# Optimization experiments

Measured on AMD Instinct MI355X. Metric: run time of the kernel, lower is better.

Reference implementation:

```python
import jax, jax.numpy as jnp
import numpy as np

B, S, D, H = 8, 2048, 1024, 8
CHUNK = D // H
SCALE = float(D) ** (-0.5)  # key_dim ** -0.5, key_dim == num_units here
LN_EPS = 1e-5


def setup_inputs() -> dict:
    key = jax.random.key(0)
    ks = jax.random.split(key, 9)
    s = 0.02
    return {
        "query": jax.random.normal(ks[0], (B, S, D), jnp.float32),
        "keys": jax.random.normal(ks[1], (B, S, D), jnp.float32),
        "Wq": jax.random.normal(ks[2], (D, D), jnp.float32) * s,  # torch Linear weight [out,in]
        "Wk": jax.random.normal(ks[3], (D, D), jnp.float32) * s,
        "Wv": jax.random.normal(ks[4], (D, D), jnp.float32) * s,
        "Wp": jax.random.normal(ks[5], (D, D), jnp.float32) * s,
        "bp": jnp.zeros((D,), jnp.float32),
        "ln_gamma": jnp.ones((D,), jnp.float32),
        "ln_beta": jnp.zeros((D,), jnp.float32),
    }


def reference(query, keys, Wq, Wk, Wv, Wp, bp, ln_gamma, ln_beta):
    # Linear layers (no bias on q/k/v): y = x @ W.T
    Q = jnp.einsum("bsd,ed->bse", query, Wq)
    K = jnp.einsum("bsd,ed->bse", keys, Wk)
    V = jnp.einsum("bsd,ed->bse", keys, Wv)
    # Faithful to original: raw view to [B*h, S, chunk] (no transpose head split)
    Qh = Q.reshape(B * H, S, CHUNK)
    Kh = K.reshape(B * H, S, CHUNK)
    Vh = V.reshape(B * H, S, CHUNK)
    # scores [B*h, S, S], scale, softmax (is_masked=False, dropout_p=0)
    att = jnp.einsum("gqc,gkc->gqk", Qh, Kh) * SCALE
    att = jax.nn.softmax(att, axis=-1)
    ctx = jnp.einsum("gqk,gkc->gqc", att, Vh).reshape(B, S, D)
    # output projection + residual + LayerNorm
    out = jnp.einsum("bsd,ed->bse", ctx, Wp) + bp
    out = out + query
    mu = jnp.mean(out, axis=-1, keepdims=True)
    var = jnp.mean(jnp.square(out - mu), axis=-1, keepdims=True)
    out = (out - mu) * jax.lax.rsqrt(var + LN_EPS) * ln_gamma + ln_beta
    return out
```

## Files before the change

kernel.cpp:

```cpp
#include <hip/hip_runtime.h>

typedef __bf16 bf16x8 __attribute__((ext_vector_type(8)));
typedef float f32x4 __attribute__((ext_vector_type(4)));
typedef float f32x16 __attribute__((ext_vector_type(16)));
typedef unsigned uint2e __attribute__((ext_vector_type(2)));

#define SCLOG 0.04508422f

__device__ __forceinline__ unsigned short f2bf(float f) {
  union { float f; unsigned int u; } v;
  v.f = f;
  unsigned int u = v.u;
  u += 0x7fffu + ((u >> 16) & 1u);
  return (unsigned short)(u >> 16);
}

__device__ __forceinline__ void gld_lds16(const void* g, void* l) {
  __builtin_amdgcn_global_load_lds(
      (const __attribute__((address_space(1))) void*)g,
      (__attribute__((address_space(3))) void*)l, 16, 0, 0);
}

__global__ __launch_bounds__(256) void convert_kernel(
    const float* __restrict__ q, const float* __restrict__ k,
    const float* __restrict__ wq, const float* __restrict__ wk,
    const float* __restrict__ wv, const float* __restrict__ wp,
    unsigned short* __restrict__ qb, unsigned short* __restrict__ kb,
    unsigned short* __restrict__ Wqkv, unsigned short* __restrict__ Wpb) {
  size_t i = (size_t)blockIdx.x * 256 + threadIdx.x;
  const float* src; unsigned short* dst; size_t off;
  if (i < 4194304)      { src = q;  dst = qb;             off = i; }
  else if (i < 8388608) { src = k;  dst = kb;             off = i - 4194304; }
  else if (i < 8650752) { src = wq; dst = Wqkv;           off = i - 8388608; }
  else if (i < 8912896) { src = wk; dst = Wqkv + 1048576; off = i - 8650752; }
  else if (i < 9175040) { src = wv; dst = Wqkv + 2097152; off = i - 8912896; }
  else                  { src = wp; dst = Wpb;            off = i - 9175040; }
  float4 v = ((const float4*)src)[off];
  ushort4 o;
  o.x = f2bf(v.x); o.y = f2bf(v.y); o.z = f2bf(v.z); o.w = f2bf(v.w);
  ((ushort4*)dst)[off] = o;
}

#define QKV_BAR __builtin_amdgcn_s_barrier()
#define QKV_LGKM asm volatile("s_waitcnt lgkmcnt(0)" ::: "memory")

#define QKV_STG(lc, h, srcb, s)                                               \
  gld_lds16((srcb) + (size_t)(s) * 128 + gro0, (lc) + (h) * 16384 + d0);      \
  gld_lds16((srcb) + (size_t)(s) * 128 + gro1, (lc) + (h) * 16384 + d0 + 1024);

#define QKV_RDA(I0)                                                           \
  _Pragma("unroll") for (int i4 = 0; i4 < 4; ++i4) {                          \
    af[i4][0] = *(const bf16x8*)(tb + rbA + ((I0) + i4) * 2048 + cx0);        \
    af[i4][1] = *(const bf16x8*)(tb + rbA + ((I0) + i4) * 2048 + cx1);        \
  }

#define QKV_RDB(JP)                                                           \
  _Pragma("unroll") for (int j2 = 0; j2 < 2; ++j2) {                          \
    bfr[JP][j2][0] = *(const bf16x8*)(tb + rbB + ((JP) * 2 + j2) * 2048 + cx0); \
    bfr[JP][j2][1] = *(const bf16x8*)(tb + rbB + ((JP) * 2 + j2) * 2048 + cx1); \
  }

#define QKV_MM(I0, JP)                                                        \
  _Pragma("unroll") for (int i4 = 0; i4 < 4; ++i4)                            \
  _Pragma("unroll") for (int j2 = 0; j2 < 2; ++j2)                            \
  _Pragma("unroll") for (int kk = 0; kk < 2; ++kk)                            \
    acc[(I0) + i4][(JP) * 2 + j2] = __builtin_amdgcn_mfma_f32_16x16x32_bf16(  \
        af[i4][kk], bfr[JP][j2][kk], acc[(I0) + i4][(JP) * 2 + j2], 0, 0, 0);

__global__ __launch_bounds__(512, 2) void gemm_qkv8_kernel(
    const unsigned short* __restrict__ qb,
    const unsigned short* __restrict__ kb,
    const unsigned short* __restrict__ W,
    unsigned short* __restrict__ Qo,
    unsigned short* __restrict__ Ko,
    unsigned short* __restrict__ Vo) {
  __shared__ char lds[131072];

  const int t = threadIdx.x;
  const int lane = t & 63;
  const int w = t >> 6;
  const int fr = lane & 15;
  const int quad = lane >> 4;

  const int orig = blockIdx.x;
  const int sseq = orig >> 3;
  const int tn = sseq >> 3;
  const int tm = (orig & 7) * 8 + (sseq & 7);

  const unsigned short* Ap = (tn < 4) ? qb : kb;
  const char* aBase = (const char*)Ap + (size_t)(tm * 256) * 2048;
  const char* bBase = (const char*)W + (size_t)(tn * 256) * 2048;

  const int wm2 = w >> 2, wn4 = w & 3;

  const size_t gro0 = (size_t)(w * 16 + (lane >> 3)) * 2048 + (size_t)(((lane & 7) ^ (lane >> 3)) << 4);
  const size_t gro1 = gro0 + 8 * 2048;
  const int d0 = w * 2048 + lane * 16;

  const int rbA = (wm2 * 128 + fr) * 128;
  const int rbB = 32768 + (wn4 * 64 + fr) * 128;
  const int cx0 = (quad * 16) ^ ((fr & 7) << 4);
  const int cx1 = cx0 ^ 64;

  f32x4 acc[8][4];
#pragma unroll
  for (int i = 0; i < 8; ++i)
#pragma unroll
    for (int j = 0; j < 4; ++j) acc[i][j] = (f32x4){0.f, 0.f, 0.f, 0.f};

#pragma unroll
  for (int s = 0; s < 2; ++s) {
    char* lc = lds + s * 65536;
    QKV_STG(lc, 0, aBase, s);
    QKV_STG(lc, 1, aBase + 262144, s);
    QKV_STG(lc + 32768, 0, bBase, s);
    QKV_STG(lc + 32768, 1, bBase + 262144, s);
  }
  asm volatile("s_waitcnt vmcnt(8)" ::: "memory");
  QKV_BAR;

#pragma unroll 1
  for (int kt = 0; kt < 16; ++kt) {
    const char* tb = lds + (kt & 1) * 65536;
    char* lc = lds + (kt & 1) * 65536;
    const int s = kt + 2;
    bf16x8 af[4][2], bfr[2][2][2];

    QKV_RDA(0);
    QKV_RDB(0);
    QKV_BAR; QKV_LGKM;
    __builtin_amdgcn_s_setprio(1);
    QKV_MM(0, 0);
    __builtin_amdgcn_s_setprio(0);
    QKV_BAR;

    QKV_RDB(1);
    QKV_BAR; QKV_LGKM;
    __builtin_amdgcn_s_setprio(1);
    QKV_MM(0, 1);
    __builtin_amdgcn_s_setprio(0);
    QKV_BAR;

    QKV_RDA(4);
    if (s < 16) {
      QKV_STG(lc + 32768, 0, bBase, s);
      QKV_STG(lc + 32768, 1, bBase + 262144, s);
    }
    QKV_BAR; QKV_LGKM;
    __builtin_amdgcn_s_setprio(1);
    QKV_MM(4, 1);
    __builtin_amdgcn_s_setprio(0);
    QKV_BAR;

    if (s < 16) {
      QKV_STG(lc, 0, aBase, s);
      QKV_STG(lc, 1, aBase + 262144, s);
    }
    QKV_BAR;
    __builtin_amdgcn_s_setprio(1);
    QKV_MM(4, 0);
    __builtin_amdgcn_s_setprio(0);
    if (kt <= 13)      { asm volatile("s_waitcnt vmcnt(8)" ::: "memory"); }
    else if (kt == 14) { asm volatile("s_waitcnt vmcnt(0)" ::: "memory"); }
    if (kt < 15) QKV_BAR;
  }

  const int sel = tn >> 2;
  unsigned short* Out = sel == 0 ? Qo : (sel == 1 ? Ko : Vo);
  const float osc = (sel == 0) ? SCLOG : 1.f;
  const int row0 = tm * 256 + wm2 * 128 + quad * 4;
  const int col0 = (tn & 3) * 256 + wn4 * 64 + fr;
#pragma unroll
  for (int i = 0; i < 8; ++i)
#pragma unroll
    for (int j = 0; j < 4; ++j)
#pragma unroll
      for (int r = 0; r < 4; ++r)
        Out[(size_t)(row0 + i * 16 + r) * 1024 + col0 + j * 16] = f2bf(acc[i][j][r] * osc);
}

__global__ __launch_bounds__(256) void vtrans_kernel(
    const unsigned short* __restrict__ V, unsigned short* __restrict__ Vt) {
  __shared__ unsigned short T[128 * 136];
  const int g  = blockIdx.x >> 4;
  const int kt = blockIdx.x & 15;
  const unsigned short* Vg = V + (size_t)g * 262144 + (size_t)kt * 128 * 128;
  unsigned short* Vtg = Vt + (size_t)g * 262144 + kt * 128;
  const int t = threadIdx.x;
#pragma unroll
  for (int it = 0; it < 8; it++) {
    int seg = t + it * 256;
    int k  = seg >> 4;
    int c8 = (seg & 15) << 3;
    uint4 a = *(const uint4*)(Vg + k * 128 + c8);
    unsigned short* Tp = &T[c8 * 136 + k];
    Tp[0 * 136] = (unsigned short)(a.x & 0xffff);
    Tp[1 * 136] = (unsigned short)(a.x >> 16);
    Tp[2 * 136] = (unsigned short)(a.y & 0xffff);
    Tp[3 * 136] = (unsigned short)(a.y >> 16);
    Tp[4 * 136] = (unsigned short)(a.z & 0xffff);
    Tp[5 * 136] = (unsigned short)(a.z >> 16);
    Tp[6 * 136] = (unsigned short)(a.w & 0xffff);
    Tp[7 * 136] = (unsigned short)(a.w >> 16);
  }
  __syncthreads();
#pragma unroll
  for (int it = 0; it < 8; it++) {
    int seg = t + it * 256;
    int c  = seg >> 4;
    int k8 = (seg & 15) << 3;
    uint4 o = *(const uint4*)&T[c * 136 + k8];
    *(uint4*)(Vtg + (size_t)c * 2048 + k8) = o;
  }
}

#define PACK_HALF(EX, KSBASE)                                                  \
    _Pragma("unroll")                                                          \
    for (int c2 = 0; c2 < 2; c2++)                                             \
      _Pragma("unroll")                                                        \
      for (int e = 0; e < 2; e++) {                                            \
        unsigned ua, ub;                                                       \
        asm("v_cvt_pk_bf16_f32 %0, %1, %2" : "=v"(ua)                          \
            : "v"(EX[8 * c2 + 2 * e]), "v"(EX[8 * c2 + 2 * e + 1]));           \
        asm("v_cvt_pk_bf16_f32 %0, %1, %2" : "=v"(ub)                          \
            : "v"(EX[8 * c2 + 4 + 2 * e]), "v"(EX[8 * c2 + 4 + 2 * e + 1]));   \
        uint2e rr = __builtin_amdgcn_permlane32_swap(ua, ub, false, false);    \
        if (e == 0) { paw[(KSBASE) + c2].x = rr[0]; paw[(KSBASE) + c2].z = rr[1]; } \
        else        { paw[(KSBASE) + c2].y = rr[0]; paw[(KSBASE) + c2].w = rr[1]; } \
      }

#define ATTN_TILE(KSH, VSH, KST, VST, PREF)                                    \
  {                                                                            \
    if (PREF) {                                                                \
      gld_lds16(kp + kS0, (KST) + kD0);                                        \
      gld_lds16(kp + kS1, (KST) + kD1);                                        \
      gld_lds16(vp + vS0, (VST) + vD0);                                        \
      gld_lds16(vp + vS1, (VST) + vD1);                                        \
      kp += 8192; vp += 64;                                                    \
    }                                                                          \
    f32x16 s0, s1;                                                             \
    _Pragma("unroll")                                                          \
    for (int r = 0; r < 16; r++) { s0[r] = 0.f; s1[r] = 0.f; }                 \
    {                                                                          \
      bf16x8 kf[8];                                                            \
      _Pragma("unroll")                                                        \
      for (int ks = 0; ks < 8; ks++)                                           \
        kf[ks] = *(const bf16x8*)((KSH) + kb0 + kOf[ks]);                      \
      _Pragma("unroll")                                                        \
      for (int ks = 0; ks < 8; ks++)                                           \
        s0 = __builtin_amdgcn_mfma_f32_32x32x16_bf16(kf[ks], qf[ks], s0, 0, 0, 0); \
    }                                                                          \
    {                                                                          \
      bf16x8 kf[8];                                                            \
      _Pragma("unroll")                                                        \
      for (int ks = 0; ks < 8; ks++)                                           \
        kf[ks] = *(const bf16x8*)((KSH) + kb0 + 8192 + kOf[ks]);               \
      _Pragma("unroll")                                                        \
      for (int ks = 0; ks < 8; ks++)                                           \
        s1 = __builtin_amdgcn_mfma_f32_32x32x16_bf16(kf[ks], qf[ks], s1, 0, 0, 0); \
    }                                                                          \
    float ex0[16], ex1[16];                                                    \
    _Pragma("unroll")                                                          \
    for (int r = 0; r < 16; r++) {                                             \
      ex0[r] = __builtin_amdgcn_exp2f(fminf(s0[r], 30.f));                     \
      ex1[r] = __builtin_amdgcn_exp2f(fminf(s1[r], 30.f));                     \
      lp += ex0[r] + ex1[r];                                                   \
    }                                                                          \
    uint4 paw[4];                                                              \
    PACK_HALF(ex0, 0)                                                          \
    PACK_HALF(ex1, 2)                                                          \
    _Pragma("unroll")                                                          \
    for (int cb = 0; cb < 4; cb++) {                                           \
      _Pragma("unroll")                                                        \
      for (int ks = 0; ks < 4; ks++) {                                         \
        bf16x8 vf = *(const bf16x8*)((VSH) + cb * 4096 + vOf[ks]);             \
        bf16x8 pa8 = __builtin_bit_cast(bf16x8, paw[ks]);                      \
        O[cb] = __builtin_amdgcn_mfma_f32_32x32x16_bf16(pa8, vf, O[cb], 0, 0, 0); \
      }                                                                        \
    }                                                                          \
    __syncthreads();                                                           \
  }

__global__ __launch_bounds__(512, 1) void attn_kernel(
    const unsigned short* __restrict__ Q,
    const unsigned short* __restrict__ K,
    const unsigned short* __restrict__ Vt,
    unsigned short* __restrict__ ctx) {
  __shared__ unsigned char smem[65536];

  const int bid = blockIdx.x;
  const int g  = (bid & 7) * 8 + (bid >> 6);
  const int qt = (bid >> 3) & 7;
  const unsigned short* Qg = Q + (size_t)g * 262144 + (size_t)qt * 32768;
  const unsigned short* Kg = K + (size_t)g * 262144;
  const unsigned short* Vg = Vt + (size_t)g * 262144;

  const int t    = threadIdx.x;
  const int lane = t & 63;
  const int wv   = t >> 6;
  const int col  = lane & 31;
  const int hi   = lane >> 5;
  const int qrow = wv * 32 + col;

  int kOf[8];
#pragma unroll
  for (int ks = 0; ks < 8; ks++) {
    int c = ks * 2 + hi;
    kOf[ks] = ((c & 8) | ((c ^ (col & 7)) & 7)) << 4;
  }
  const int kb0 = col * 256;
  int vOf[4];
#pragma unroll
  for (int ks = 0; ks < 4; ks++) {
    int c = ks * 2 + hi;
    vOf[ks] = col * 128 + (((c ^ (col & 7)) & 7) << 4);
  }
  int kS0, kS1, kD0, kD1, vS0, vS1, vD0, vD1;
  {
    int seg0 = t, seg1 = t + 512;
    int r0 = seg0 >> 4, p0 = seg0 & 15, c0 = (p0 & 8) | ((p0 ^ r0) & 7);
    int r1 = seg1 >> 4, p1 = seg1 & 15, c1 = (p1 & 8) | ((p1 ^ r1) & 7);
    kS0 = r0 * 128 + c0 * 8;  kD0 = seg0 * 16;
    kS1 = r1 * 128 + c1 * 8;  kD1 = seg1 * 16;
    int vr0 = seg0 >> 3, vp0 = seg0 & 7, vc0 = vp0 ^ (vr0 & 7);
    int vr1 = seg1 >> 3, vp1 = seg1 & 7, vc1 = vp1 ^ (vr1 & 7);
    vS0 = vr0 * 2048 + vc0 * 8;  vD0 = seg0 * 16;
    vS1 = vr1 * 2048 + vc1 * 8;  vD1 = seg1 * 16;
  }

#pragma unroll
  for (int it = 0; it < 8; it++) {
    int seg = t + it * 512;
    int r = seg >> 4, p = seg & 15;
    int c = (p & 8) | ((p ^ r) & 7);
    gld_lds16(Qg + r * 128 + c * 8, smem + seg * 16);
  }
  __syncthreads();
  bf16x8 qf[8];
#pragma unroll
  for (int ks = 0; ks < 8; ks++) {
    int c = ks * 2 + hi;
    int p = (c & 8) | ((c ^ (qrow & 7)) & 7);
    qf[ks] = *(const bf16x8*)(smem + qrow * 256 + p * 16);
  }
  __syncthreads();

  gld_lds16(Kg + kS0, smem + kD0);
  gld_lds16(Kg + kS1, smem + kD1);
  gld_lds16(Vg + vS0, smem + 32768 + vD0);
  gld_lds16(Vg + vS1, smem + 32768 + vD1);
  __syncthreads();

  const unsigned short* kp = Kg + 8192;
  const unsigned short* vp = Vg + 64;

  f32x16 O[4];
#pragma unroll
  for (int cb = 0; cb < 4; cb++)
#pragma unroll
    for (int r = 0; r < 16; r++) O[cb][r] = 0.f;
  float lp = 0.f;

  unsigned char* B0K = smem;
  unsigned char* B1K = smem + 16384;
  unsigned char* B0V = smem + 32768;
  unsigned char* B1V = smem + 49152;

#pragma unroll 1
  for (int kt2 = 0; kt2 < 16; kt2++) {
    ATTN_TILE(B0K, B0V, B1K, B1V, 1);
    ATTN_TILE(B1K, B1V, B0K, B0V, (kt2 < 15));
  }

  lp += __shfl_xor(lp, 32);
  float* linv_arr = (float*)smem;
  linv_arr[wv * 32 + col] = 1.f / lp;
  float4 li[4];
#pragma unroll
  for (int rq = 0; rq < 4; rq++)
    li[rq] = *(const float4*)&linv_arr[wv * 32 + rq * 8 + hi * 4];

  unsigned short* Cg = ctx + (size_t)g * 262144 + (size_t)qt * 32768;
#pragma unroll
  for (int cb = 0; cb < 4; cb++)
#pragma unroll
    for (int rq = 0; rq < 4; rq++)
#pragma unroll
      for (int j = 0; j < 4; j++) {
        int row = wv * 32 + rq * 8 + hi * 4 + j;
        Cg[(size_t)row * 128 + cb * 32 + col] = f2bf(O[cb][rq * 4 + j] * li[rq][j]);
      }
}

__global__ __launch_bounds__(256) void gemm_proj_kernel(
    const unsigned short* __restrict__ A,
    const unsigned short* __restrict__ W,
    const float* __restrict__ bp,
    const float* __restrict__ qres,
    float* __restrict__ out) {
  __shared__ unsigned short Alds[128 * 32];
  __shared__ unsigned short Blds[128 * 32];
  const int t   = threadIdx.x;
  const int bid = blockIdx.x;
  const int tn  = bid % 8;
  const int tm  = bid / 8;
  const unsigned short* Bptr = W + (size_t)tn * 128 * 1024;

  const int lane = t & 63;
  const int wv   = t >> 6;
  const int wm   = (wv >> 1) * 64;
  const int wn   = (wv & 1) * 64;
  const int fr   = lane & 15;
  const int kq   = (lane >> 4) * 8;

  f32x4 acc[4][4];
#pragma unroll
  for (int i = 0; i < 4; i++)
#pragma unroll
    for (int j = 0; j < 4; j++) acc[i][j] = (f32x4){0.f, 0.f, 0.f, 0.f};

  const int sr = t >> 2;
  const int sc = (t & 3) << 3;
  const unsigned short* gA = A + (size_t)(tm * 128 + sr) * 1024 + sc;
  const unsigned short* gB = Bptr + (size_t)sr * 1024 + sc;
  unsigned short* lA = Alds + t * 8;
  unsigned short* lB = Blds + t * 8;

  for (int k0 = 0; k0 < 1024; k0 += 32) {
    gld_lds16(gA, lA);
    gld_lds16(gA + 64 * 1024, lA + 64 * 32);
    gld_lds16(gB, lB);
    gld_lds16(gB + 64 * 1024, lB + 64 * 32);
    gA += 32; gB += 32;
    __syncthreads();
    bf16x8 af[4], bfr[4];
#pragma unroll
    for (int i = 0; i < 4; i++) {
      af[i]  = *(const bf16x8*)&Alds[(wm + i * 16 + fr) * 32 + kq];
      bfr[i] = *(const bf16x8*)&Blds[(wn + i * 16 + fr) * 32 + kq];
    }
#pragma unroll
    for (int i = 0; i < 4; i++)
#pragma unroll
      for (int j = 0; j < 4; j++)
        acc[i][j] = __builtin_amdgcn_mfma_f32_16x16x32_bf16(af[i], bfr[j], acc[i][j], 0, 0, 0);
    __syncthreads();
  }

  const int quad = lane >> 4;
  const int cc   = lane & 15;
#pragma unroll
  for (int i = 0; i < 4; i++)
#pragma unroll
    for (int j = 0; j < 4; j++)
#pragma unroll
      for (int r = 0; r < 4; r++) {
        int row = tm * 128 + wm + i * 16 + quad * 4 + r;
        int col = tn * 128 + wn + j * 16 + cc;
        out[(size_t)row * 1024 + col] =
            acc[i][j][r] + bp[col] + qres[(size_t)row * 1024 + col];
      }
}

__global__ __launch_bounds__(256) void ln_kernel(float* __restrict__ out,
                                                 const float* __restrict__ gamma,
                                                 const float* __restrict__ beta) {
  __shared__ float red[8];
  const int row = blockIdx.x;
  float* p = out + (size_t)row * 1024;
  const int t = threadIdx.x;
  float4 v = ((const float4*)p)[t];
  float s  = v.x + v.y + v.z + v.w;
  float s2 = v.x * v.x + v.y * v.y + v.z * v.z + v.w * v.w;
#pragma unroll
  for (int off = 1; off < 64; off <<= 1) {
    s  += __shfl_xor(s, off);
    s2 += __shfl_xor(s2, off);
  }
  const int wv = t >> 6;
  if ((t & 63) == 0) { red[wv] = s; red[4 + wv] = s2; }
  __syncthreads();
  float S  = red[0] + red[1] + red[2] + red[3];
  float S2 = red[4] + red[5] + red[6] + red[7];
  float mu  = S * (1.f / 1024.f);
  float var = S2 * (1.f / 1024.f) - mu * mu;
  float rstd = rsqrtf(var + 1e-5f);
  float4 gm = ((const float4*)gamma)[t];
  float4 bt = ((const float4*)beta)[t];
  v.x = (v.x - mu) * rstd * gm.x + bt.x;
  v.y = (v.y - mu) * rstd * gm.y + bt.y;
  v.z = (v.z - mu) * rstd * gm.z + bt.z;
  v.w = (v.w - mu) * rstd * gm.w + bt.w;
  ((float4*)p)[t] = v;
}

extern "C" void kernel_launch(void* const* d_in, const int* in_sizes, int n_in,
                              void* d_out, int out_size, void* d_ws, size_t ws_size,
                              hipStream_t stream) {
  const float* query = (const float*)d_in[0];
  const float* keys  = (const float*)d_in[1];
  const float* Wq    = (const float*)d_in[2];
  const float* Wk    = (const float*)d_in[3];
  const float* Wv    = (const float*)d_in[4];
  const float* Wp    = (const float*)d_in[5];
  const float* bp    = (const float*)d_in[6];
  const float* gamma = (const float*)d_in[7];
  const float* beta  = (const float*)d_in[8];
  float* out = (float*)d_out;

  unsigned short* ws   = (unsigned short*)d_ws;
  unsigned short* qb   = ws;
  unsigned short* kb   = ws + 16777216;
  unsigned short* Wqkv = ws + 33554432;
  unsigned short* Wpb  = ws + 36700160;
  unsigned short* Qb   = ws + 37748736;
  unsigned short* Kb   = ws + 54525952;
  unsigned short* Vb   = ws + 71303168;
  unsigned short* Vtb  = kb;
  unsigned short* ctx  = qb;

  convert_kernel<<<36864, 256, 0, stream>>>(query, keys, Wq, Wk, Wv, Wp, qb, kb, Wqkv, Wpb);
  gemm_qkv8_kernel<<<768, 512, 0, stream>>>(qb, kb, Wqkv, Qb, Kb, Vb);
  vtrans_kernel<<<1024, 256, 0, stream>>>(Vb, Vtb);
  attn_kernel<<<512, 512, 0, stream>>>(Qb, Kb, Vtb, ctx);
  gemm_proj_kernel<<<1024, 256, 0, stream>>>(ctx, Wpb, bp, query, out);
  ln_kernel<<<16384, 256, 0, stream>>>(out, gamma, beta);
}
```

Before: 523.7 us.

## Reuse pipelined 256x256 QKV GEMM for output projection; widen attention LDS swizzle

Result: faster. 507.1 us (-3.2%).

```diff
diff --git a/kernel.cpp b/kernel.cpp
--- a/kernel.cpp
+++ b/kernel.cpp
@@ -67,6 +67,75 @@
     acc[(I0) + i4][(JP) * 2 + j2] = __builtin_amdgcn_mfma_f32_16x16x32_bf16(  \
         af[i4][kk], bfr[JP][j2][kk], acc[(I0) + i4][(JP) * 2 + j2], 0, 0, 0);
 
+#define QKV_KLOOP                                                             \
+  _Pragma("unroll")                                                           \
+  for (int s = 0; s < 2; ++s) {                                               \
+    char* lc = lds + s * 65536;                                               \
+    QKV_STG(lc, 0, aBase, s);                                                 \
+    QKV_STG(lc, 1, aBase + 262144, s);                                        \
+    QKV_STG(lc + 32768, 0, bBase, s);                                         \
+    QKV_STG(lc + 32768, 1, bBase + 262144, s);                                \
+  }                                                                           \
+  asm volatile("s_waitcnt vmcnt(8)" ::: "memory");                            \
+  QKV_BAR;                                                                    \
+  _Pragma("unroll 1")                                                         \
+  for (int kt = 0; kt < 16; ++kt) {                                           \
+    const char* tb = lds + (kt & 1) * 65536;                                  \
+    char* lc = lds + (kt & 1) * 65536;                                        \
+    const int s = kt + 2;                                                     \
+    bf16x8 af[4][2], bfr[2][2][2];                                            \
+    QKV_RDA(0);                                                               \
+    QKV_RDB(0);                                                               \
+    QKV_BAR; QKV_LGKM;                                                        \
+    __builtin_amdgcn_s_setprio(1);                                            \
+    QKV_MM(0, 0);                                                             \
+    __builtin_amdgcn_s_setprio(0);                                            \
+    QKV_BAR;                                                                  \
+    QKV_RDB(1);                                                               \
+    QKV_BAR; QKV_LGKM;                                                        \
+    __builtin_amdgcn_s_setprio(1);                                            \
+    QKV_MM(0, 1);                                                             \
+    __builtin_amdgcn_s_setprio(0);                                            \
+    QKV_BAR;                                                                  \
+    QKV_RDA(4);                                                               \
+    if (s < 16) {                                                             \
+      QKV_STG(lc + 32768, 0, bBase, s);                                       \
+      QKV_STG(lc + 32768, 1, bBase + 262144, s);                              \
+    }                                                                         \
+    QKV_BAR; QKV_LGKM;                                                        \
+    __builtin_amdgcn_s_setprio(1);                                            \
+    QKV_MM(4, 1);                                                             \
+    __builtin_amdgcn_s_setprio(0);                                            \
+    QKV_BAR;                                                                  \
+    if (s < 16) {                                                             \
+      QKV_STG(lc, 0, aBase, s);                                               \
+      QKV_STG(lc, 1, aBase + 262144, s);                                      \
+    }                                                                         \
+    QKV_BAR;                                                                  \
+    __builtin_amdgcn_s_setprio(1);                                            \
+    QKV_MM(4, 0);                                                             \
+    __builtin_amdgcn_s_setprio(0);                                            \
+    if (kt <= 13)      { asm volatile("s_waitcnt vmcnt(8)" ::: "memory"); }   \
+    else if (kt == 14) { asm volatile("s_waitcnt vmcnt(0)" ::: "memory"); }   \
+    if (kt < 15) QKV_BAR;                                                     \
+  }
+
+#define QKV_COMMON_DECLS                                                      \
+  const int t = threadIdx.x;                                                  \
+  const int lane = t & 63;                                                    \
+  const int w = t >> 6;                                                       \
+  const int fr = lane & 15;                                                   \
+  const int quad = lane >> 4;                                                 \
+  const int wm2 = w >> 2, wn4 = w & 3;                                        \
+  const size_t gro0 = (size_t)(w * 16 + (lane >> 3)) * 2048 +                 \
+                      (size_t)(((lane & 7) ^ (lane >> 3)) << 4);              \
+  const size_t gro1 = gro0 + 8 * 2048;                                        \
+  const int d0 = w * 2048 + lane * 16;                                        \
+  const int rbA = (wm2 * 128 + fr) * 128;                                     \
+  const int rbB = 32768 + (wn4 * 64 + fr) * 128;                              \
+  const int cx0 = (quad * 16) ^ ((fr & 7) << 4);                              \
+  const int cx1 = cx0 ^ 64;
+
 __global__ __launch_bounds__(512, 2) void gemm_qkv8_kernel(
     const unsigned short* __restrict__ qb,
     const unsigned short* __restrict__ kb,
@@ -75,12 +144,7 @@
     unsigned short* __restrict__ Ko,
     unsigned short* __restrict__ Vo) {
   __shared__ char lds[131072];
-
-  const int t = threadIdx.x;
-  const int lane = t & 63;
-  const int w = t >> 6;
-  const int fr = lane & 15;
-  const int quad = lane >> 4;
+  QKV_COMMON_DECLS
 
   const int orig = blockIdx.x;
   const int sseq = orig >> 3;
@@ -91,79 +155,13 @@
   const char* aBase = (const char*)Ap + (size_t)(tm * 256) * 2048;
   const char* bBase = (const char*)W + (size_t)(tn * 256) * 2048;
 
-  const int wm2 = w >> 2, wn4 = w & 3;
-
-  const size_t gro0 = (size_t)(w * 16 + (lane >> 3)) * 2048 + (size_t)(((lane & 7) ^ (lane >> 3)) << 4);
-  const size_t gro1 = gro0 + 8 * 2048;
-  const int d0 = w * 2048 + lane * 16;
-
-  const int rbA = (wm2 * 128 + fr) * 128;
-  const int rbB = 32768 + (wn4 * 64 + fr) * 128;
-  const int cx0 = (quad * 16) ^ ((fr & 7) << 4);
-  const int cx1 = cx0 ^ 64;
-
   f32x4 acc[8][4];
 #pragma unroll
   for (int i = 0; i < 8; ++i)
 #pragma unroll
     for (int j = 0; j < 4; ++j) acc[i][j] = (f32x4){0.f, 0.f, 0.f, 0.f};
 
-#pragma unroll
-  for (int s = 0; s < 2; ++s) {
-    char* lc = lds + s * 65536;
-    QKV_STG(lc, 0, aBase, s);
-    QKV_STG(lc, 1, aBase + 262144, s);
-    QKV_STG(lc + 32768, 0, bBase, s);
-    QKV_STG(lc + 32768, 1, bBase + 262144, s);
-  }
-  asm volatile("s_waitcnt vmcnt(8)" ::: "memory");
-  QKV_BAR;
-
-#pragma unroll 1
-  for (int kt = 0; kt < 16; ++kt) {
-    const char* tb = lds + (kt & 1) * 65536;
-    char* lc = lds + (kt & 1) * 65536;
-    const int s = kt + 2;
-    bf16x8 af[4][2], bfr[2][2][2];
-
-    QKV_RDA(0);
-    QKV_RDB(0);
-    QKV_BAR; QKV_LGKM;
-    __builtin_amdgcn_s_setprio(1);
-    QKV_MM(0, 0);
-    __builtin_amdgcn_s_setprio(0);
-    QKV_BAR;
-
-    QKV_RDB(1);
-    QKV_BAR; QKV_LGKM;
-    __builtin_amdgcn_s_setprio(1);
-    QKV_MM(0, 1);
-    __builtin_amdgcn_s_setprio(0);
-    QKV_BAR;
-
-    QKV_RDA(4);
-    if (s < 16) {
-      QKV_STG(lc + 32768, 0, bBase, s);
-      QKV_STG(lc + 32768, 1, bBase + 262144, s);
-    }
-    QKV_BAR; QKV_LGKM;
-    __builtin_amdgcn_s_setprio(1);
-    QKV_MM(4, 1);
-    __builtin_amdgcn_s_setprio(0);
-    QKV_BAR;
-
-    if (s < 16) {
-      QKV_STG(lc, 0, aBase, s);
-      QKV_STG(lc, 1, aBase + 262144, s);
-    }
-    QKV_BAR;
-    __builtin_amdgcn_s_setprio(1);
-    QKV_MM(4, 0);
-    __builtin_amdgcn_s_setprio(0);
-    if (kt <= 13)      { asm volatile("s_waitcnt vmcnt(8)" ::: "memory"); }
-    else if (kt == 14) { asm volatile("s_waitcnt vmcnt(0)" ::: "memory"); }
-    if (kt < 15) QKV_BAR;
-  }
+  QKV_KLOOP
 
   const int sel = tn >> 2;
   unsigned short* Out = sel == 0 ? Qo : (sel == 1 ? Ko : Vo);
@@ -177,6 +175,47 @@
 #pragma unroll
       for (int r = 0; r < 4; ++r)
         Out[(size_t)(row0 + i * 16 + r) * 1024 + col0 + j * 16] = f2bf(acc[i][j][r] * osc);
+}
+
+__global__ __launch_bounds__(512, 2) void gemm_proj8_kernel(
+    const unsigned short* __restrict__ A,
+    const unsigned short* __restrict__ W,
+    const float* __restrict__ bp,
+    const float* __restrict__ qres,
+    float* __restrict__ out) {
+  __shared__ char lds[131072];
+  QKV_COMMON_DECLS
+
+  const int orig = blockIdx.x;
+  const int sseq = orig >> 3;
+  const int tn = sseq >> 3;
+  const int tm = (orig & 7) * 8 + (sseq & 7);
+
+  const char* aBase = (const char*)A + (size_t)(tm * 256) * 2048;
+  const char* bBase = (const char*)W + (size_t)(tn * 256) * 2048;
+
+  f32x4 acc[8][4];
+#pragma unroll
+  for (int i = 0; i < 8; ++i)
+#pragma unroll
+    for (int j = 0; j < 4; ++j) acc[i][j] = (f32x4){0.f, 0.f, 0.f, 0.f};
+
+  QKV_KLOOP
+
+  const int row0 = tm * 256 + wm2 * 128 + quad * 4;
+  const int col0 = tn * 256 + wn4 * 64 + fr;
+#pragma unroll
+  for (int i = 0; i < 8; ++i)
+#pragma unroll
+    for (int j = 0; j < 4; ++j) {
+      const int col = col0 + j * 16;
+      const float bpc = bp[col];
+#pragma unroll
+      for (int r = 0; r < 4; ++r) {
+        const size_t idx = (size_t)(row0 + i * 16 + r) * 1024 + col;
+        out[idx] = acc[i][j][r] + bpc + qres[idx];
+      }
+    }
 }
 
 __global__ __launch_bounds__(256) void vtrans_kernel(
@@ -306,33 +345,33 @@
 #pragma unroll
   for (int ks = 0; ks < 8; ks++) {
     int c = ks * 2 + hi;
-    kOf[ks] = ((c & 8) | ((c ^ (col & 7)) & 7)) << 4;
+    kOf[ks] = (c ^ (col & 15)) << 4;
   }
   const int kb0 = col * 256;
   int vOf[4];
 #pragma unroll
   for (int ks = 0; ks < 4; ks++) {
     int c = ks * 2 + hi;
-    vOf[ks] = col * 128 + (((c ^ (col & 7)) & 7) << 4);
+    vOf[ks] = col * 128 + (((c ^ (col & 7) ^ ((col >> 3) & 1)) & 7) << 4);
   }
   int kS0, kS1, kD0, kD1, vS0, vS1, vD0, vD1;
   {
     int seg0 = t, seg1 = t + 512;
-    int r0 = seg0 >> 4, p0 = seg0 & 15, c0 = (p0 & 8) | ((p0 ^ r0) & 7);
-    int r1 = seg1 >> 4, p1 = seg1 & 15, c1 = (p1 & 8) | ((p1 ^ r1) & 7);
-    kS0 = r0 * 128 + c0 * 8;  kD0 = seg0 * 16;
-    kS1 = r1 * 128 + c1 * 8;  kD1 = seg1 * 16;
-    int vr0 = seg0 >> 3, vp0 = seg0 & 7, vc0 = vp0 ^ (vr0 & 7);
-    int vr1 = seg1 >> 3, vp1 = seg1 & 7, vc1 = vp1 ^ (vr1 & 7);
-    vS0 = vr0 * 2048 + vc0 * 8;  vD0 = seg0 * 16;
-    vS1 = vr1 * 2048 + vc1 * 8;  vD1 = seg1 * 16;
+    int r0 = seg0 >> 4, p0 = seg0 & 15;
+    int r1 = seg1 >> 4, p1 = seg1 & 15;
+    kS0 = r0 * 128 + (p0 ^ (r0 & 15)) * 8;  kD0 = seg0 * 16;
+    kS1 = r1 * 128 + (p1 ^ (r1 & 15)) * 8;  kD1 = seg1 * 16;
+    int vr0 = seg0 >> 3, vp0 = seg0 & 7;
+    int vr1 = seg1 >> 3, vp1 = seg1 & 7;
+    vS0 = vr0 * 2048 + ((vp0 ^ (vr0 & 7) ^ ((vr0 >> 3) & 1)) & 7) * 8;  vD0 = seg0 * 16;
+    vS1 = vr1 * 2048 + ((vp1 ^ (vr1 & 7) ^ ((vr1 >> 3) & 1)) & 7) * 8;  vD1 = seg1 * 16;
   }
 
 #pragma unroll
   for (int it = 0; it < 8; it++) {
     int seg = t + it * 512;
     int r = seg >> 4, p = seg & 15;
-    int c = (p & 8) | ((p ^ r) & 7);
+    int c = p ^ (r & 15);
     gld_lds16(Qg + r * 128 + c * 8, smem + seg * 16);
   }
   __syncthreads();
@@ -340,7 +379,7 @@
 #pragma unroll
   for (int ks = 0; ks < 8; ks++) {
     int c = ks * 2 + hi;
-    int p = (c & 8) | ((c ^ (qrow & 7)) & 7);
+    int p = c ^ (qrow & 15);
     qf[ks] = *(const bf16x8*)(smem + qrow * 256 + p * 16);
   }
   __syncthreads();
@@ -389,76 +428,6 @@
       for (int j = 0; j < 4; j++) {
         int row = wv * 32 + rq * 8 + hi * 4 + j;
         Cg[(size_t)row * 128 + cb * 32 + col] = f2bf(O[cb][rq * 4 + j] * li[rq][j]);
-      }
-}
-
-__global__ __launch_bounds__(256) void gemm_proj_kernel(
-    const unsigned short* __restrict__ A,
-    const unsigned short* __restrict__ W,
-    const float* __restrict__ bp,
-    const float* __restrict__ qres,
-    float* __restrict__ out) {
-  __shared__ unsigned short Alds[128 * 32];
-  __shared__ unsigned short Blds[128 * 32];
-  const int t   = threadIdx.x;
-  const int bid = blockIdx.x;
-  const int tn  = bid % 8;
-  const int tm  = bid / 8;
-  const unsigned short* Bptr = W + (size_t)tn * 128 * 1024;
-
-  const int lane = t & 63;
-  const int wv   = t >> 6;
-  const int wm   = (wv >> 1) * 64;
-  const int wn   = (wv & 1) * 64;
-  const int fr   = lane & 15;
-  const int kq   = (lane >> 4) * 8;
-
-  f32x4 acc[4][4];
-#pragma unroll
-  for (int i = 0; i < 4; i++)
-#pragma unroll
-    for (int j = 0; j < 4; j++) acc[i][j] = (f32x4){0.f, 0.f, 0.f, 0.f};
-
-  const int sr = t >> 2;
-  const int sc = (t & 3) << 3;
-  const unsigned short* gA = A + (size_t)(tm * 128 + sr) * 1024 + sc;
-  const unsigned short* gB = Bptr + (size_t)sr * 1024 + sc;
-  unsigned short* lA = Alds + t * 8;
-  unsigned short* lB = Blds + t * 8;
-
-  for (int k0 = 0; k0 < 1024; k0 += 32) {
-    gld_lds16(gA, lA);
-    gld_lds16(gA + 64 * 1024, lA + 64 * 32);
-    gld_lds16(gB, lB);
-    gld_lds16(gB + 64 * 1024, lB + 64 * 32);
-    gA += 32; gB += 32;
-    __syncthreads();
-    bf16x8 af[4], bfr[4];
-#pragma unroll
-    for (int i = 0; i < 4; i++) {
-      af[i]  = *(const bf16x8*)&Alds[(wm + i * 16 + fr) * 32 + kq];
-      bfr[i] = *(const bf16x8*)&Blds[(wn + i * 16 + fr) * 32 + kq];
-    }
-#pragma unroll
-    for (int i = 0; i < 4; i++)
-#pragma unroll
-      for (int j = 0; j < 4; j++)
-        acc[i][j] = __builtin_amdgcn_mfma_f32_16x16x32_bf16(af[i], bfr[j], acc[i][j], 0, 0, 0);
-    __syncthreads();
-  }
-
-  const int quad = lane >> 4;
-  const int cc   = lane & 15;
-#pragma unroll
-  for (int i = 0; i < 4; i++)
-#pragma unroll
-    for (int j = 0; j < 4; j++)
-#pragma unroll
-      for (int r = 0; r < 4; r++) {
-        int row = tm * 128 + wm + i * 16 + quad * 4 + r;
-        int col = tn * 128 + wn + j * 16 + cc;
-        out[(size_t)row * 1024 + col] =
-            acc[i][j][r] + bp[col] + qres[(size_t)row * 1024 + col];
       }
 }
 
@@ -523,6 +492,6 @@
   gemm_qkv8_kernel<<<768, 512, 0, stream>>>(qb, kb, Wqkv, Qb, Kb, Vb);
   vtrans_kernel<<<1024, 256, 0, stream>>>(Vb, Vtb);
   attn_kernel<<<512, 512, 0, stream>>>(Qb, Kb, Vtb, ctx);
-  gemm_proj_kernel<<<1024, 256, 0, stream>>>(ctx, Wpb, bp, query, out);
+  gemm_proj8_kernel<<<256, 512, 0, stream>>>(ctx, Wpb, bp, query, out);
   ln_kernel<<<16384, 256, 0, stream>>>(out, gamma, beta);
 }
```
